# Optimization experiments

Hardware: AMD Instinct MI355X
Metric: run time of the kernel (lower is better)

Reference implementation:

```python
import jax, jax.numpy as jnp
import numpy as np

S = 4096      # sequence length
E = 256       # embedding_dim
H = 256       # hidden_dim // 2 (per direction)
T = 16        # tagset size
V = 100000    # vocab size
START = 14
STOP = 15
NEG = -10000.0


def setup_inputs() -> dict:
    key = jax.random.key(0)
    ks = jax.random.split(key, 16)
    trans = jax.random.normal(ks[12], (T, T), jnp.float32)
    trans = trans.at[START, :].set(NEG).at[:, STOP].set(NEG)
    return {
        "sentence": jax.random.randint(ks[0], (S,), 0, V),
        "embed": jax.random.normal(ks[1], (V, E), jnp.float32),
        "W_ih_f": jax.random.normal(ks[2], (4 * H, E), jnp.float32) * 0.05,
        "W_hh_f": jax.random.normal(ks[3], (4 * H, H), jnp.float32) * 0.05,
        "b_ih_f": jax.random.normal(ks[4], (4 * H,), jnp.float32) * 0.05,
        "b_hh_f": jax.random.normal(ks[5], (4 * H,), jnp.float32) * 0.05,
        "W_ih_b": jax.random.normal(ks[6], (4 * H, E), jnp.float32) * 0.05,
        "W_hh_b": jax.random.normal(ks[7], (4 * H, H), jnp.float32) * 0.05,
        "b_ih_b": jax.random.normal(ks[8], (4 * H,), jnp.float32) * 0.05,
        "b_hh_b": jax.random.normal(ks[9], (4 * H,), jnp.float32) * 0.05,
        "W_out": jax.random.normal(ks[10], (T, 2 * H), jnp.float32) * 0.05,
        "b_out": jax.random.normal(ks[11], (T,), jnp.float32) * 0.05,
        "transitions": trans,
        "h0": jax.random.normal(ks[13], (2, H), jnp.float32),
        "c0": jax.random.normal(ks[14], (2, H), jnp.float32),
    }


def _lstm(x, h0, c0, W_ih, W_hh, b_ih, b_hh):
    """Single-direction LSTM over x:[S,E]; PyTorch gate order i,f,g,o."""
    b = b_ih + b_hh
    xg = x @ W_ih.T + b  # [S, 4H] precompute input contribution

    def step(carry, xt):
        h, c = carry
        g = xt + h @ W_hh.T
        i, f, gg, o = jnp.split(g, 4)
        i = jax.nn.sigmoid(i)
        f = jax.nn.sigmoid(f)
        gg = jnp.tanh(gg)
        o = jax.nn.sigmoid(o)
        c = f * c + i * gg
        h = o * jnp.tanh(c)
        return (h, c), h

    _, hs = jax.lax.scan(step, (h0, c0), xg)
    return hs  # [S, H]


def reference(sentence, embed, W_ih_f, W_hh_f, b_ih_f, b_hh_f,
              W_ih_b, W_hh_b, b_ih_b, b_hh_b, W_out, b_out,
              transitions, h0, c0):
    x = embed[sentence]  # [S, E]
    hf = _lstm(x, h0[0], c0[0], W_ih_f, W_hh_f, b_ih_f, b_hh_f)
    hb = _lstm(x[::-1], h0[1], c0[1], W_ih_b, W_hh_b, b_ih_b, b_hh_b)[::-1]
    feats = jnp.concatenate([hf, hb], axis=-1) @ W_out.T + b_out  # [S, T]

    # CRF forward algorithm (log partition). transitions[i, j] = score j -> i.
    alpha0 = jnp.full((T,), NEG, feats.dtype).at[START].set(0.0)

    def crf_step(alpha, emit):
        a = jax.nn.logsumexp(alpha[None, :] + transitions, axis=1) + emit
        return a, None

    alpha, _ = jax.lax.scan(crf_step, alpha0, feats)
    return jax.nn.logsumexp(alpha + transitions[STOP])
```

## Files before the change

### kernel.cpp

```cpp
#include <hip/hip_runtime.h>
#include <hip/hip_bf16.h>

#define S 4096
#define E 256
#define HH 256
#define TT 16
#define NEG_ -10000.0f
#define START_ 14
#define STOP_ 15

__device__ __forceinline__ float fast_exp(float x) {
    return __builtin_amdgcn_exp2f(x * 1.4426950408889634f);
}
__device__ __forceinline__ float fast_log(float x) {
    return 0.6931471805599453f * __builtin_amdgcn_logf(x);
}

__global__ __launch_bounds__(64) void quant4_kernel(
    const float* __restrict__ Wf, const float* __restrict__ Wb,
    const float* __restrict__ h0,
    int* __restrict__ wq4, float* __restrict__ wscale,
    int* __restrict__ hq0p, float* __restrict__ sh0)
{
    int blk = blockIdx.x, lane = threadIdx.x;
    const float* src;
    int* dst;
    float* scl;
    bool fixed = false;
    if (blk < 2048) {
        int d = blk >> 10, r = blk & 1023;
        src = (d == 0 ? Wf : Wb) + (size_t)r * 256;
        dst = wq4 + ((size_t)(d * 1024 + r)) * 32;
        scl = wscale + (d * 1024 + r);
    } else {
        int d = blk - 2048;
        src = h0 + (size_t)d * 256;
        dst = hq0p + d * 32;
        scl = sh0 + d;
        fixed = true;
    }
    float4 a = make_float4(0.f, 0.f, 0.f, 0.f), b = a;
    if (lane < 32) {
        a = ((const float4*)src)[2 * lane];
        b = ((const float4*)src)[2 * lane + 1];
    }
    float f[8] = {a.x, a.y, a.z, a.w, b.x, b.y, b.z, b.w};
    float m = 0.f;
    #pragma unroll
    for (int k = 0; k < 8; ++k) m = fmaxf(m, fabsf(f[k]));
    #pragma unroll
    for (int off = 1; off < 64; off <<= 1) m = fmaxf(m, __shfl_xor(m, off, 64));
    m = fmaxf(m, 1e-20f);
    float inv = fixed ? 7.0f : (7.0f / m);
    if (lane < 32) {
        int dw = 0;
        #pragma unroll
        for (int k = 0; k < 8; ++k) {
            int q = __float2int_rn(f[k] * inv);
            q = max(-8, min(7, q));
            dw |= (q & 0xF) << (4 * k);
        }
        dst[lane] = dw;
    }
    if (lane == 0) *scl = fixed ? (1.0f / 7.0f) : (m / 7.0f);
}

__global__ __launch_bounds__(256) void xg_kernel(
    const int* __restrict__ sent, const float* __restrict__ embed,
    const float* __restrict__ Wf, const float* __restrict__ bihf, const float* __restrict__ bhhf,
    const float* __restrict__ Wb, const float* __restrict__ bihb, const float* __restrict__ bhhb,
    float* __restrict__ xg)
{
    const int dir = blockIdx.y;
    const int t0 = blockIdx.x * 16;
    const int tid = threadIdx.x;
    const float* W = dir ? Wb : Wf;
    __shared__ float xt[16][256];
    for (int tt = 0; tt < 16; ++tt) {
        int t = t0 + tt;
        int pos = dir ? (S - 1 - t) : t;
        int w = sent[pos];
        xt[tt][tid] = embed[(size_t)w * 256 + tid];
    }
    __syncthreads();
    float acc[4][16];
    #pragma unroll
    for (int rc = 0; rc < 4; ++rc)
        #pragma unroll
        for (int tt = 0; tt < 16; ++tt) acc[rc][tt] = 0.f;
    for (int e = 0; e < 256; ++e) {
        float xv[16];
        #pragma unroll
        for (int tt = 0; tt < 16; ++tt) xv[tt] = xt[tt][e];
        #pragma unroll
        for (int rc = 0; rc < 4; ++rc) {
            float w = W[(size_t)(rc * 256 + tid) * 256 + e];
            #pragma unroll
            for (int tt = 0; tt < 16; ++tt) acc[rc][tt] += w * xv[tt];
        }
    }
    const float* bih = dir ? bihb : bihf;
    const float* bhh = dir ? bhhb : bhhf;
    float b0 = bih[0 * 256 + tid] + bhh[0 * 256 + tid];
    float b1 = bih[1 * 256 + tid] + bhh[1 * 256 + tid];
    float b2 = bih[2 * 256 + tid] + bhh[2 * 256 + tid];
    float b3 = bih[3 * 256 + tid] + bhh[3 * 256 + tid];
    #pragma unroll
    for (int tt = 0; tt < 16; ++tt) {
        float4 v;
        v.x = acc[0][tt] + b0;
        v.y = acc[1][tt] + b1;
        v.z = acc[2][tt] + b2;
        v.w = acc[3][tt] + b3;
        ((float4*)(xg + ((size_t)dir * S + (t0 + tt)) * 1024))[tid] = v;
    }
}

#define D8(a,w,h) "v_dot8_i32_i4 " a ", " w ", " h ", " a "\n\t"
#define CH(H0,H1,H2,H3, I0,I1,I2,I3, F0,F1,F2,F3, G0,G1,G2,G3, O0,O1,O2,O3) \
 D8("v192",I0,H0) D8("v193",F0,H0) D8("v194",G0,H0) D8("v195",O0,H0) \
 D8("v192",I1,H1) D8("v193",F1,H1) D8("v194",G1,H1) D8("v195",O1,H1) \
 D8("v192",I2,H2) D8("v193",F2,H2) D8("v194",G2,H2) D8("v195",O2,H2) \
 D8("v192",I3,H3) D8("v193",F3,H3) D8("v194",G3,H3) D8("v195",O3,H3)

#define LSTM_BODY(XI, XF, XG, XO, NQUAD) \
  "global_load_dwordx4 " NQUAD ", v204, %[sxg]\n\t" \
  "ds_read_b128 v[160:163], v206\n\t" \
  "ds_read_b128 v[164:167], v206 offset:16\n\t" \
  "ds_read_b128 v[168:171], v206 offset:32\n\t" \
  "ds_read_b128 v[172:175], v206 offset:48\n\t" \
  "ds_read_b128 v[176:179], v206 offset:64\n\t" \
  "ds_read_b128 v[180:183], v206 offset:80\n\t" \
  "ds_read_b128 v[184:187], v206 offset:96\n\t" \
  "ds_read_b128 v[188:191], v206 offset:112\n\t" \
  "v_mov_b32 v192, 0\n\t" \
  "v_mov_b32 v193, 0\n\t" \
  "v_mov_b32 v194, 0\n\t" \
  "v_mov_b32 v195, 0\n\t" \
  "s_waitcnt lgkmcnt(7)\n\t" \
  CH("v160","v161","v162","v163", "v32","v33","v34","v35", "v64","v65","v66","v67", "v96","v97","v98","v99", "v128","v129","v130","v131") \
  "s_waitcnt lgkmcnt(6)\n\t" \
  CH("v164","v165","v166","v167", "v36","v37","v38","v39", "v68","v69","v70","v71", "v100","v101","v102","v103", "v132","v133","v134","v135") \
  "s_waitcnt lgkmcnt(5)\n\t" \
  CH("v168","v169","v170","v171", "v40","v41","v42","v43", "v72","v73","v74","v75", "v104","v105","v106","v107", "v136","v137","v138","v139") \
  "s_waitcnt lgkmcnt(4)\n\t" \
  CH("v172","v173","v174","v175", "v44","v45","v46","v47", "v76","v77","v78","v79", "v108","v109","v110","v111", "v140","v141","v142","v143") \
  "s_waitcnt lgkmcnt(3)\n\t" \
  CH("v176","v177","v178","v179", "v48","v49","v50","v51", "v80","v81","v82","v83", "v112","v113","v114","v115", "v144","v145","v146","v147") \
  "s_waitcnt lgkmcnt(2)\n\t" \
  CH("v180","v181","v182","v183", "v52","v53","v54","v55", "v84","v85","v86","v87", "v116","v117","v118","v119", "v148","v149","v150","v151") \
  "s_waitcnt lgkmcnt(1)\n\t" \
  CH("v184","v185","v186","v187", "v56","v57","v58","v59", "v88","v89","v90","v91", "v120","v121","v122","v123", "v152","v153","v154","v155") \
  "s_waitcnt lgkmcnt(0)\n\t" \
  CH("v188","v189","v190","v191", "v60","v61","v62","v63", "v92","v93","v94","v95", "v124","v125","v126","v127", "v156","v157","v158","v159") \
  "v_cvt_f32_i32 v208, v192\n\t" \
  "v_cvt_f32_i32 v209, v193\n\t" \
  "v_cvt_f32_i32 v210, v194\n\t" \
  "v_cvt_f32_i32 v211, v195\n\t" \
  "s_waitcnt vmcnt(2)\n\t" \
  "v_fma_f32 v212, %[sci], v208, " XI "\n\t" \
  "v_fma_f32 v213, %[scf], v209, " XF "\n\t" \
  "v_fma_f32 v214, %[scg], v210, " XG "\n\t" \
  "v_fma_f32 v215, %[sco], v211, " XO "\n\t" \
  "v_mul_f32 v208, %[nk], v212\n\t" \
  "v_mul_f32 v209, %[nk], v213\n\t" \
  "v_mul_f32 v211, %[nk], v215\n\t" \
  "v_med3_f32 v214, v214, %[ncl], %[pcl]\n\t" \
  "v_mul_f32 v210, %[k2], v214\n\t" \
  "v_exp_f32 v208, v208\n\t" \
  "v_exp_f32 v209, v209\n\t" \
  "v_exp_f32 v211, v211\n\t" \
  "v_exp_f32 v210, v210\n\t" \
  "s_nop 1\n\t" \
  "v_add_f32 v212, 1.0, v208\n\t" \
  "v_add_f32 v213, 1.0, v209\n\t" \
  "v_add_f32 v215, 1.0, v211\n\t" \
  "v_add_f32 v216, 1.0, v210\n\t" \
  "v_add_f32 v217, -1.0, v210\n\t" \
  "v_rcp_f32 v212, v212\n\t" \
  "v_rcp_f32 v213, v213\n\t" \
  "v_rcp_f32 v215, v215\n\t" \
  "v_rcp_f32 v216, v216\n\t" \
  "s_nop 1\n\t" \
  "v_mul_f32 v217, v217, v216\n\t" \
  "v_mul_f32 v220, v213, v220\n\t" \
  "v_fmac_f32 v220, v212, v217\n\t" \
  "v_med3_f32 v208, v220, %[ncl], %[pcl]\n\t" \
  "v_mul_f32 v208, %[k2], v208\n\t" \
  "v_exp_f32 v208, v208\n\t" \
  "s_nop 1\n\t" \
  "v_add_f32 v209, -1.0, v208\n\t" \
  "v_add_f32 v210, 1.0, v208\n\t" \
  "v_rcp_f32 v210, v210\n\t" \
  "s_nop 1\n\t" \
  "v_mul_f32 v209, v209, v210\n\t" \
  "v_mul_f32 v218, v215, v209\n\t" \
  "global_store_dword v205, v218, %[shs]\n\t" \
  "v_mul_f32 v208, %[c7], v218\n\t" \
  "v_rndne_f32 v208, v208\n\t" \
  "v_cvt_i32_f32 v208, v208\n\t" \
  "v_and_b32 v208, 15, v208\n\t" \
  "v_lshlrev_b32 v208, v225, v208\n\t" \
  "s_nop 1\n\t" \
  "v_mov_b32_dpp v209, v208 quad_perm:[1,0,3,2] row_mask:0xf bank_mask:0xf\n\t" \
  "v_or_b32 v208, v208, v209\n\t" \
  "s_nop 1\n\t" \
  "v_mov_b32_dpp v209, v208 quad_perm:[2,3,0,1] row_mask:0xf bank_mask:0xf\n\t" \
  "v_or_b32 v208, v208, v209\n\t" \
  "ds_write_b16 v207, v208\n\t" \
  "v_add_u32 v204, 0x1000, v204\n\t" \
  "v_add_u32 v205, 0x400, v205\n\t" \
  "v_xor_b32 v206, 0x80, v206\n\t" \
  "v_xor_b32 v207, 0x80, v207\n\t" \
  "s_waitcnt lgkmcnt(0)\n\t" \
  "s_barrier\n\t"

__global__ __launch_bounds__(256, 1) void lstm_kernel(
    const float* __restrict__ xg, const int* __restrict__ wq4,
    const float* __restrict__ wscale, const int* __restrict__ hq0p,
    const float* __restrict__ c0, float* __restrict__ hs)
{
    const int d = blockIdx.x;
    const int t = threadIdx.x;

    __shared__ alignas(16) int hq4buf[256];

    const int*   wq_d = wq4 + (size_t)d * 32768;
    const float* xg_d = xg + (size_t)d * S * 1024;
    float*       hs_d = hs + (size_t)d * S * 256;
    const float sci = wscale[d * 1024 + t]       * (1.0f / 7.0f);
    const float scf = wscale[d * 1024 + 256 + t] * (1.0f / 7.0f);
    const float scg = wscale[d * 1024 + 512 + t] * (1.0f / 7.0f);
    const float sco = wscale[d * 1024 + 768 + t] * (1.0f / 7.0f);
    const float c0v = c0[d * 256 + t];
    const int h0v = hq0p[d * 32 + (t & 31)];
    const unsigned h0a = (t < 32) ? (unsigned)t * 4u : (512u + (unsigned)(t & 63) * 4u);
    const unsigned xai = (unsigned)t * 16u;
    const unsigned hsi = (unsigned)t * 4u;
    const unsigned wad = ((t & 3) == 0) ? (128u + (unsigned)(t >> 1))
                                        : (512u + (unsigned)t * 2u);
    const unsigned voW = (unsigned)t * 128u;
    const unsigned shf = (unsigned)(t & 3) * 4u;
    const float nk = -1.4426950408889634f;
    const float k2 = 2.8853900817779268f;
    const float c7 = 7.0f;
    const float ncl = -30.0f, pcl = 30.0f;
    const unsigned lds_keep = (unsigned)(size_t)&hq4buf[0];
    int cnt = S / 2;

    asm volatile(
        "v_mov_b32 v204, %[xai]\n\t"
        "v_mov_b32 v205, %[hsi]\n\t"
        "v_mov_b32 v206, 0\n\t"
        "v_mov_b32 v207, %[wad]\n\t"
        "v_mov_b32 v220, %[c0v]\n\t"
        "v_mov_b32 v221, %[sci]\n\t"
        "v_mov_b32 v222, %[scf]\n\t"
        "v_mov_b32 v223, %[scg]\n\t"
        "v_mov_b32 v224, %[sco]\n\t"
        "v_mov_b32 v225, %[shf]\n\t"
        "ds_write_b32 %[h0a], %[h0v]\n\t"
        "v_mov_b32 v208, %[voW]\n\t"
        "global_load_dwordx4 v[32:35], v208, %[swq]\n\t"
        "global_load_dwordx4 v[36:39], v208, %[swq] offset:16\n\t"
        "global_load_dwordx4 v[40:43], v208, %[swq] offset:32\n\t"
        "global_load_dwordx4 v[44:47], v208, %[swq] offset:48\n\t"
        "global_load_dwordx4 v[48:51], v208, %[swq] offset:64\n\t"
        "global_load_dwordx4 v[52:55], v208, %[swq] offset:80\n\t"
        "global_load_dwordx4 v[56:59], v208, %[swq] offset:96\n\t"
        "global_load_dwordx4 v[60:63], v208, %[swq] offset:112\n\t"
        "v_add_u32 v208, 0x8000, v208\n\t"
        "global_load_dwordx4 v[64:67], v208, %[swq]\n\t"
        "global_load_dwordx4 v[68:71], v208, %[swq] offset:16\n\t"
        "global_load_dwordx4 v[72:75], v208, %[swq] offset:32\n\t"
        "global_load_dwordx4 v[76:79], v208, %[swq] offset:48\n\t"
        "global_load_dwordx4 v[80:83], v208, %[swq] offset:64\n\t"
        "global_load_dwordx4 v[84:87], v208, %[swq] offset:80\n\t"
        "global_load_dwordx4 v[88:91], v208, %[swq] offset:96\n\t"
        "global_load_dwordx4 v[92:95], v208, %[swq] offset:112\n\t"
        "v_add_u32 v208, 0x8000, v208\n\t"
        "global_load_dwordx4 v[96:99],   v208, %[swq]\n\t"
        "global_load_dwordx4 v[100:103], v208, %[swq] offset:16\n\t"
        "global_load_dwordx4 v[104:107], v208, %[swq] offset:32\n\t"
        "global_load_dwordx4 v[108:111], v208, %[swq] offset:48\n\t"
        "global_load_dwordx4 v[112:115], v208, %[swq] offset:64\n\t"
        "global_load_dwordx4 v[116:119], v208, %[swq] offset:80\n\t"
        "global_load_dwordx4 v[120:123], v208, %[swq] offset:96\n\t"
        "global_load_dwordx4 v[124:127], v208, %[swq] offset:112\n\t"
        "v_add_u32 v208, 0x8000, v208\n\t"
        "global_load_dwordx4 v[128:131], v208, %[swq]\n\t"
        "global_load_dwordx4 v[132:135], v208, %[swq] offset:16\n\t"
        "global_load_dwordx4 v[136:139], v208, %[swq] offset:32\n\t"
        "global_load_dwordx4 v[140:143], v208, %[swq] offset:48\n\t"
        "global_load_dwordx4 v[144:147], v208, %[swq] offset:64\n\t"
        "global_load_dwordx4 v[148:151], v208, %[swq] offset:80\n\t"
        "global_load_dwordx4 v[152:155], v208, %[swq] offset:96\n\t"
        "global_load_dwordx4 v[156:159], v208, %[swq] offset:112\n\t"
        "global_load_dwordx4 v[196:199], v204, %[sxg]\n\t"
        "v_add_u32 v204, 0x1000, v204\n\t"
        "s_waitcnt vmcnt(0) lgkmcnt(0)\n\t"
        "s_barrier\n\t"
        "Llstm%=:\n\t"
        LSTM_BODY("v196", "v197", "v198", "v199", "v[200:203]")
        LSTM_BODY("v200", "v201", "v202", "v203", "v[196:199]")
        "s_add_i32 %[cnt], %[cnt], -1\n\t"
        "s_cmp_lg_u32 %[cnt], 0\n\t"
        "s_cbranch_scc1 Llstm%=\n\t"
        : [cnt] "+s"(cnt)
        : [sxg] "s"(xg_d), [shs] "s"(hs_d), [swq] "s"(wq_d),
          [xai] "v"(xai), [hsi] "v"(hsi), [wad] "v"(wad),
          [c0v] "v"(c0v), [h0a] "v"(h0a), [h0v] "v"(h0v),
          [sci] "v"(sci), [scf] "v"(scf), [scg] "v"(scg), [sco] "v"(sco),
          [nk] "v"(nk), [k2] "v"(k2), [c7] "v"(c7),
          [ncl] "v"(ncl), [pcl] "v"(pcl),
          [voW] "v"(voW), [shf] "v"(shf), [keep] "v"(lds_keep)
        : "memory", "scc",
          "v32","v33","v34","v35","v36","v37","v38","v39",
          "v40","v41","v42","v43","v44","v45","v46","v47",
          "v48","v49","v50","v51","v52","v53","v54","v55",
          "v56","v57","v58","v59","v60","v61","v62","v63",
          "v64","v65","v66","v67","v68","v69","v70","v71",
          "v72","v73","v74","v75","v76","v77","v78","v79",
          "v80","v81","v82","v83","v84","v85","v86","v87",
          "v88","v89","v90","v91","v92","v93","v94","v95",
          "v96","v97","v98","v99","v100","v101","v102","v103",
          "v104","v105","v106","v107","v108","v109","v110","v111",
          "v112","v113","v114","v115","v116","v117","v118","v119",
          "v120","v121","v122","v123","v124","v125","v126","v127",
          "v128","v129","v130","v131","v132","v133","v134","v135",
          "v136","v137","v138","v139","v140","v141","v142","v143",
          "v144","v145","v146","v147","v148","v149","v150","v151",
          "v152","v153","v154","v155","v156","v157","v158","v159",
          "v160","v161","v162","v163","v164","v165","v166","v167",
          "v168","v169","v170","v171","v172","v173","v174","v175",
          "v176","v177","v178","v179","v180","v181","v182","v183",
          "v184","v185","v186","v187","v188","v189","v190","v191",
          "v192","v193","v194","v195","v196","v197","v198","v199",
          "v200","v201","v202","v203","v204","v205","v206","v207",
          "v208","v209","v210","v211","v212","v213","v214","v215",
          "v216","v217","v218","v219","v220","v221","v222","v223",
          "v224","v225");
}

__global__ __launch_bounds__(256) void feats_kernel(
    const float* __restrict__ hs, const float* __restrict__ Wout,
    const float* __restrict__ bout, float* __restrict__ feats)
{
    __shared__ float Wl[16][513];
    int tid = threadIdx.x;
    for (int i = tid; i < 16 * 512; i += 256) Wl[i >> 9][i & 511] = Wout[i];
    __syncthreads();
    int tt = tid >> 4, tag = tid & 15;
    int tcur = blockIdx.x * 16 + tt;
    const float* hf = hs + (size_t)tcur * 256;
    const float* hb = hs + (size_t)S * 256 + (size_t)(S - 1 - tcur) * 256;
    float acc = bout[tag];
    for (int k = 0; k < 256; ++k) acc += Wl[tag][k] * hf[k];
    for (int k = 0; k < 256; ++k) acc += Wl[tag][256 + k] * hb[k];
    feats[(size_t)tcur * 16 + tag] = acc;
}

__global__ __launch_bounds__(256) void crf_chunk_kernel(
    const float* __restrict__ feats, const float* __restrict__ trans,
    float* __restrict__ P)
{
    int chunk = blockIdx.x;
    int tid = threadIdx.x;
    int i = tid >> 4, jj = tid & 15;
    __shared__ float Mt[2][16][17];
    float tr[16];
    #pragma unroll
    for (int k = 0; k < 16; ++k) tr[k] = trans[i * 16 + k];
    int t0 = chunk * 64;
    float emit = feats[(size_t)t0 * 16 + i];
    Mt[0][jj][i] = tr[jj] + emit;
    __syncthreads();
    int cur = 0;
    float em_next = feats[(size_t)(t0 + 1) * 16 + i];
    for (int s = 1; s < 64; ++s) {
        float em = em_next;
        if (s + 1 < 64) em_next = feats[(size_t)(t0 + s + 1) * 16 + i];
        float v[16];
        #pragma unroll
        for (int k = 0; k < 16; ++k) v[k] = tr[k] + Mt[cur][jj][k];
        float m = v[0];
        #pragma unroll
        for (int k = 1; k < 16; ++k) m = fmaxf(m, v[k]);
        float ssum = 0.f;
        #pragma unroll
        for (int k = 0; k < 16; ++k) ssum += fast_exp(v[k] - m);
        float nv = em + m + fast_log(ssum);
        Mt[cur ^ 1][jj][i] = nv;
        cur ^= 1;
        __syncthreads();
    }
    P[((size_t)chunk * 16 + i) * 16 + jj] = Mt[cur][jj][i];
}

__global__ __launch_bounds__(256) void crf_fold_kernel(
    const float* __restrict__ P, const float* __restrict__ trans,
    float* __restrict__ out)
{
    int tid = threadIdx.x;
    int i = tid >> 4, jj = tid & 15;
    __shared__ float alpha[16];
    if (tid < 16) alpha[tid] = (tid == START_) ? 0.0f : NEG_;
    __syncthreads();
    for (int cc = 0; cc < 64; ++cc) {
        float pv = P[((size_t)cc * 16 + i) * 16 + jj];
        float v = pv + alpha[jj];
        float m = v;
        #pragma unroll
        for (int off = 1; off < 16; off <<= 1) m = fmaxf(m, __shfl_xor(m, off, 64));
        float e = fast_exp(v - m);
        #pragma unroll
        for (int off = 1; off < 16; off <<= 1) e += __shfl_xor(e, off, 64);
        float nv = m + fast_log(e);
        __syncthreads();
        if (jj == 0) alpha[i] = nv;
        __syncthreads();
    }
    if (tid < 16) {
        float v = alpha[tid] + trans[STOP_ * 16 + tid];
        float m = v;
        #pragma unroll
        for (int off = 1; off < 16; off <<= 1) m = fmaxf(m, __shfl_xor(m, off, 64));
        float e = fast_exp(v - m);
        #pragma unroll
        for (int off = 1; off < 16; off <<= 1) e += __shfl_xor(e, off, 64);
        if (tid == 0) out[0] = m + fast_log(e);
    }
}

extern "C" void kernel_launch(void* const* d_in, const int* in_sizes, int n_in,
                              void* d_out, int out_size, void* d_ws, size_t ws_size,
                              hipStream_t stream) {
    const int*   sent  = (const int*)d_in[0];
    const float* embed = (const float*)d_in[1];
    const float* Wihf  = (const float*)d_in[2];
    const float* Whhf  = (const float*)d_in[3];
    const float* bihf  = (const float*)d_in[4];
    const float* bhhf  = (const float*)d_in[5];
    const float* Wihb  = (const float*)d_in[6];
    const float* Whhb  = (const float*)d_in[7];
    const float* bihb  = (const float*)d_in[8];
    const float* bhhb  = (const float*)d_in[9];
    const float* Wout  = (const float*)d_in[10];
    const float* bout  = (const float*)d_in[11];
    const float* trans = (const float*)d_in[12];
    const float* h0    = (const float*)d_in[13];
    const float* c0    = (const float*)d_in[14];
    float* out = (float*)d_out;

    char* ws = (char*)d_ws;
    constexpr size_t OFF_XG     = 0;
    constexpr size_t OFF_WQ     = OFF_XG + (size_t)2 * S * 1024 * 4;
    constexpr size_t OFF_WSCALE = OFF_WQ + (size_t)2 * 1024 * 32 * 4;
    constexpr size_t OFF_HQ0    = OFF_WSCALE + 2 * 1024 * 4;
    constexpr size_t OFF_SH0    = OFF_HQ0 + 2 * 32 * 4;
    constexpr size_t OFF_HS     = OFF_SH0 + 256;
    constexpr size_t OFF_FEATS  = OFF_HS + (size_t)2 * S * 256 * 4;
    constexpr size_t OFF_P      = OFF_FEATS + (size_t)S * 16 * 4;

    float* xg     = (float*)(ws + OFF_XG);
    int*   wq4    = (int*)(ws + OFF_WQ);
    float* wscale = (float*)(ws + OFF_WSCALE);
    int*   hq0p   = (int*)(ws + OFF_HQ0);
    float* sh0    = (float*)(ws + OFF_SH0);
    float* hs     = (float*)(ws + OFF_HS);
    float* feats  = (float*)(ws + OFF_FEATS);
    float* P      = (float*)(ws + OFF_P);

    quant4_kernel<<<dim3(2050), dim3(64), 0, stream>>>(Whhf, Whhb, h0, wq4, wscale, hq0p, sh0);
    xg_kernel<<<dim3(256, 2), dim3(256), 0, stream>>>(sent, embed, Wihf, bihf, bhhf,
                                                      Wihb, bihb, bhhb, xg);
    lstm_kernel<<<dim3(2), dim3(256), 0, stream>>>(xg, wq4, wscale, hq0p, c0, hs);
    feats_kernel<<<dim3(256), dim3(256), 0, stream>>>(hs, Wout, bout, feats);
    crf_chunk_kernel<<<dim3(64), dim3(256), 0, stream>>>(feats, trans, P);
    crf_fold_kernel<<<dim3(1), dim3(256), 0, stream>>>(P, trans, out);
}
```

Measured before the change: 2.362 ms.

## Defer hidden-state store, double-buffer LDS h, and transpose W_ih for coalesced xg

The LSTM step loop is rescheduled. The global store of h and the xg prefetch move to the top of the next iteration, the LDS h buffer is double-buffered so reads and writes alternate, and accumulator zeroing moves off the critical path. Hidden-state quantisation now uses a magic-number add instead of rndne plus cvt, and the output arrays get a one-row offset to absorb the delayed store. A new transpose kernel makes W_ih reads in xg_kernel coalesced, at the cost of an extra launch and scratch buffer.

```diff
diff --git a/kernel.cpp b/kernel.cpp
--- a/kernel.cpp
+++ b/kernel.cpp
@@ -8,6 +8,7 @@
 #define NEG_ -10000.0f
 #define START_ 14
 #define STOP_ 15
+#define DSTRIDE_F (S * 256 + 256)
 
 __device__ __forceinline__ float fast_exp(float x) {
     return __builtin_amdgcn_exp2f(x * 1.4426950408889634f);
@@ -20,12 +21,12 @@
     const float* __restrict__ Wf, const float* __restrict__ Wb,
     const float* __restrict__ h0,
     int* __restrict__ wq4, float* __restrict__ wscale,
-    int* __restrict__ hq0p, float* __restrict__ sh0)
+    int* __restrict__ hq0p)
 {
     int blk = blockIdx.x, lane = threadIdx.x;
     const float* src;
     int* dst;
-    float* scl;
+    float* scl = nullptr;
     bool fixed = false;
     if (blk < 2048) {
         int d = blk >> 10, r = blk & 1023;
@@ -36,7 +37,6 @@
         int d = blk - 2048;
         src = h0 + (size_t)d * 256;
         dst = hq0p + d * 32;
-        scl = sh0 + d;
         fixed = true;
     }
     float4 a = make_float4(0.f, 0.f, 0.f, 0.f), b = a;
@@ -62,19 +62,39 @@
         }
         dst[lane] = dw;
     }
-    if (lane == 0) *scl = fixed ? (1.0f / 7.0f) : (m / 7.0f);
+    if (!fixed && lane == 0) *scl = m / 7.0f;
+}
+
+__global__ __launch_bounds__(256) void transpose_kernel(
+    const float* __restrict__ Wf, const float* __restrict__ Wb,
+    float* __restrict__ WT)
+{
+    __shared__ float tile[32][33];
+    const int dir = blockIdx.z;
+    const float* W = dir ? Wb : Wf;
+    const int r0 = blockIdx.x * 32, e0 = blockIdx.y * 32;
+    const int tr = threadIdx.x & 31, tc = threadIdx.x >> 5;
+    #pragma unroll
+    for (int i = 0; i < 32; i += 8)
+        tile[tc + i][tr] = W[(size_t)(r0 + tc + i) * 256 + e0 + tr];
+    __syncthreads();
+    float* out = WT + (size_t)dir * 256 * 1024;
+    #pragma unroll
+    for (int i = 0; i < 32; i += 8)
+        out[(size_t)(e0 + tc + i) * 1024 + r0 + tr] = tile[tr][tc + i];
 }
 
 __global__ __launch_bounds__(256) void xg_kernel(
     const int* __restrict__ sent, const float* __restrict__ embed,
-    const float* __restrict__ Wf, const float* __restrict__ bihf, const float* __restrict__ bhhf,
-    const float* __restrict__ Wb, const float* __restrict__ bihb, const float* __restrict__ bhhb,
+    const float* __restrict__ WT,
+    const float* __restrict__ bihf, const float* __restrict__ bhhf,
+    const float* __restrict__ bihb, const float* __restrict__ bhhb,
     float* __restrict__ xg)
 {
     const int dir = blockIdx.y;
     const int t0 = blockIdx.x * 16;
     const int tid = threadIdx.x;
-    const float* W = dir ? Wb : Wf;
+    const float* Wt = WT + (size_t)dir * 256 * 1024;
     __shared__ float xt[16][256];
     for (int tt = 0; tt < 16; ++tt) {
         int t = t0 + tt;
@@ -92,9 +112,10 @@
         float xv[16];
         #pragma unroll
         for (int tt = 0; tt < 16; ++tt) xv[tt] = xt[tt][e];
+        const float* wrow = Wt + (size_t)e * 1024;
         #pragma unroll
         for (int rc = 0; rc < 4; ++rc) {
-            float w = W[(size_t)(rc * 256 + tid) * 256 + e];
+            float w = wrow[rc * 256 + tid];
             #pragma unroll
             for (int tt = 0; tt < 16; ++tt) acc[rc][tt] += w * xv[tt];
         }
@@ -124,7 +145,6 @@
  D8("v192",I3,H3) D8("v193",F3,H3) D8("v194",G3,H3) D8("v195",O3,H3)
 
 #define LSTM_BODY(XI, XF, XG, XO, NQUAD) \
-  "global_load_dwordx4 " NQUAD ", v204, %[sxg]\n\t" \
   "ds_read_b128 v[160:163], v206\n\t" \
   "ds_read_b128 v[164:167], v206 offset:16\n\t" \
   "ds_read_b128 v[168:171], v206 offset:32\n\t" \
@@ -133,10 +153,11 @@
   "ds_read_b128 v[180:183], v206 offset:80\n\t" \
   "ds_read_b128 v[184:187], v206 offset:96\n\t" \
   "ds_read_b128 v[188:191], v206 offset:112\n\t" \
-  "v_mov_b32 v192, 0\n\t" \
-  "v_mov_b32 v193, 0\n\t" \
-  "v_mov_b32 v194, 0\n\t" \
-  "v_mov_b32 v195, 0\n\t" \
+  "v_xor_b32 v206, 0x80, v206\n\t" \
+  "global_store_dword v205, v218, %[shs]\n\t" \
+  "v_add_u32 v205, 0x400, v205\n\t" \
+  "global_load_dwordx4 " NQUAD ", v204, %[sxg]\n\t" \
+  "v_add_u32 v204, 0x1000, v204\n\t" \
   "s_waitcnt lgkmcnt(7)\n\t" \
   CH("v160","v161","v162","v163", "v32","v33","v34","v35", "v64","v65","v66","v67", "v96","v97","v98","v99", "v128","v129","v130","v131") \
   "s_waitcnt lgkmcnt(6)\n\t" \
@@ -183,6 +204,7 @@
   "v_rcp_f32 v216, v216\n\t" \
   "s_nop 1\n\t" \
   "v_mul_f32 v217, v217, v216\n\t" \
+  "v_mul_f32 v219, %[c7], v215\n\t" \
   "v_mul_f32 v220, v213, v220\n\t" \
   "v_fmac_f32 v220, v212, v217\n\t" \
   "v_med3_f32 v208, v220, %[ncl], %[pcl]\n\t" \
@@ -194,13 +216,11 @@
   "v_rcp_f32 v210, v210\n\t" \
   "s_nop 1\n\t" \
   "v_mul_f32 v209, v209, v210\n\t" \
-  "v_mul_f32 v218, v215, v209\n\t" \
-  "global_store_dword v205, v218, %[shs]\n\t" \
-  "v_mul_f32 v208, %[c7], v218\n\t" \
-  "v_rndne_f32 v208, v208\n\t" \
-  "v_cvt_i32_f32 v208, v208\n\t" \
+  "v_mul_f32 v217, v219, v209\n\t" \
+  "v_add_f32 v208, 0x4b400000, v217\n\t" \
   "v_and_b32 v208, 15, v208\n\t" \
   "v_lshlrev_b32 v208, v225, v208\n\t" \
+  "v_mul_f32 v218, %[i7], v217\n\t" \
   "s_nop 1\n\t" \
   "v_mov_b32_dpp v209, v208 quad_perm:[1,0,3,2] row_mask:0xf bank_mask:0xf\n\t" \
   "v_or_b32 v208, v208, v209\n\t" \
@@ -208,10 +228,11 @@
   "v_mov_b32_dpp v209, v208 quad_perm:[2,3,0,1] row_mask:0xf bank_mask:0xf\n\t" \
   "v_or_b32 v208, v208, v209\n\t" \
   "ds_write_b16 v207, v208\n\t" \
-  "v_add_u32 v204, 0x1000, v204\n\t" \
-  "v_add_u32 v205, 0x400, v205\n\t" \
-  "v_xor_b32 v206, 0x80, v206\n\t" \
   "v_xor_b32 v207, 0x80, v207\n\t" \
+  "v_mov_b32 v192, 0\n\t" \
+  "v_mov_b32 v193, 0\n\t" \
+  "v_mov_b32 v194, 0\n\t" \
+  "v_mov_b32 v195, 0\n\t" \
   "s_waitcnt lgkmcnt(0)\n\t" \
   "s_barrier\n\t"
 
@@ -223,27 +244,28 @@
     const int d = blockIdx.x;
     const int t = threadIdx.x;
 
-    __shared__ alignas(16) int hq4buf[256];
+    __shared__ alignas(16) int hq4buf[512];
 
     const int*   wq_d = wq4 + (size_t)d * 32768;
     const float* xg_d = xg + (size_t)d * S * 1024;
-    float*       hs_d = hs + (size_t)d * S * 256;
+    float*       hs_d = hs + (size_t)d * DSTRIDE_F;
     const float sci = wscale[d * 1024 + t]       * (1.0f / 7.0f);
     const float scf = wscale[d * 1024 + 256 + t] * (1.0f / 7.0f);
     const float scg = wscale[d * 1024 + 512 + t] * (1.0f / 7.0f);
     const float sco = wscale[d * 1024 + 768 + t] * (1.0f / 7.0f);
     const float c0v = c0[d * 256 + t];
     const int h0v = hq0p[d * 32 + (t & 31)];
-    const unsigned h0a = (t < 32) ? (unsigned)t * 4u : (512u + (unsigned)(t & 63) * 4u);
+    const unsigned h0a = (t < 32) ? (unsigned)t * 4u : (1536u + (unsigned)(t & 63) * 4u);
     const unsigned xai = (unsigned)t * 16u;
     const unsigned hsi = (unsigned)t * 4u;
     const unsigned wad = ((t & 3) == 0) ? (128u + (unsigned)(t >> 1))
-                                        : (512u + (unsigned)t * 2u);
+                                        : (512u + (unsigned)((t & 255) << 2));
     const unsigned voW = (unsigned)t * 128u;
     const unsigned shf = (unsigned)(t & 3) * 4u;
     const float nk = -1.4426950408889634f;
     const float k2 = 2.8853900817779268f;
     const float c7 = 7.0f;
+    const float i7 = 1.0f / 7.0f;
     const float ncl = -30.0f, pcl = 30.0f;
     const unsigned lds_keep = (unsigned)(size_t)&hq4buf[0];
     int cnt = S / 2;
@@ -253,12 +275,13 @@
         "v_mov_b32 v205, %[hsi]\n\t"
         "v_mov_b32 v206, 0\n\t"
         "v_mov_b32 v207, %[wad]\n\t"
+        "v_mov_b32 v218, 0\n\t"
         "v_mov_b32 v220, %[c0v]\n\t"
-        "v_mov_b32 v221, %[sci]\n\t"
-        "v_mov_b32 v222, %[scf]\n\t"
-        "v_mov_b32 v223, %[scg]\n\t"
-        "v_mov_b32 v224, %[sco]\n\t"
         "v_mov_b32 v225, %[shf]\n\t"
+        "v_mov_b32 v192, 0\n\t"
+        "v_mov_b32 v193, 0\n\t"
+        "v_mov_b32 v194, 0\n\t"
+        "v_mov_b32 v195, 0\n\t"
         "ds_write_b32 %[h0a], %[h0v]\n\t"
         "v_mov_b32 v208, %[voW]\n\t"
         "global_load_dwordx4 v[32:35], v208, %[swq]\n\t"
@@ -306,12 +329,13 @@
         "s_add_i32 %[cnt], %[cnt], -1\n\t"
         "s_cmp_lg_u32 %[cnt], 0\n\t"
         "s_cbranch_scc1 Llstm%=\n\t"
+        "global_store_dword v205, v218, %[shs]\n\t"
         : [cnt] "+s"(cnt)
         : [sxg] "s"(xg_d), [shs] "s"(hs_d), [swq] "s"(wq_d),
           [xai] "v"(xai), [hsi] "v"(hsi), [wad] "v"(wad),
           [c0v] "v"(c0v), [h0a] "v"(h0a), [h0v] "v"(h0v),
           [sci] "v"(sci), [scf] "v"(scf), [scg] "v"(scg), [sco] "v"(sco),
-          [nk] "v"(nk), [k2] "v"(k2), [c7] "v"(c7),
+          [nk] "v"(nk), [k2] "v"(k2), [c7] "v"(c7), [i7] "v"(i7),
           [ncl] "v"(ncl), [pcl] "v"(pcl),
           [voW] "v"(voW), [shf] "v"(shf), [keep] "v"(lds_keep)
         : "memory", "scc",
@@ -343,7 +367,8 @@
 }
 
 __global__ __launch_bounds__(256) void feats_kernel(
-    const float* __restrict__ hs, const float* __restrict__ Wout,
+    const float* __restrict__ hsf, const float* __restrict__ hsb,
+    const float* __restrict__ Wout,
     const float* __restrict__ bout, float* __restrict__ feats)
 {
     __shared__ float Wl[16][513];
@@ -352,8 +377,8 @@
     __syncthreads();
     int tt = tid >> 4, tag = tid & 15;
     int tcur = blockIdx.x * 16 + tt;
-    const float* hf = hs + (size_t)tcur * 256;
-    const float* hb = hs + (size_t)S * 256 + (size_t)(S - 1 - tcur) * 256;
+    const float* hf = hsf + (size_t)tcur * 256;
+    const float* hb = hsb + (size_t)(S - 1 - tcur) * 256;
     float acc = bout[tag];
     for (int k = 0; k < 256; ++k) acc += Wl[tag][k] * hf[k];
     for (int k = 0; k < 256; ++k) acc += Wl[tag][256 + k] * hb[k];
@@ -457,25 +482,27 @@
     constexpr size_t OFF_WQ     = OFF_XG + (size_t)2 * S * 1024 * 4;
     constexpr size_t OFF_WSCALE = OFF_WQ + (size_t)2 * 1024 * 32 * 4;
     constexpr size_t OFF_HQ0    = OFF_WSCALE + 2 * 1024 * 4;
-    constexpr size_t OFF_SH0    = OFF_HQ0 + 2 * 32 * 4;
-    constexpr size_t OFF_HS     = OFF_SH0 + 256;
-    constexpr size_t OFF_FEATS  = OFF_HS + (size_t)2 * S * 256 * 4;
+    constexpr size_t OFF_WT     = OFF_HQ0 + 256;
+    constexpr size_t OFF_HS     = OFF_WT + (size_t)2 * 256 * 1024 * 4;
+    constexpr size_t OFF_FEATS  = OFF_HS + (size_t)2 * DSTRIDE_F * 4;
     constexpr size_t OFF_P      = OFF_FEATS + (size_t)S * 16 * 4;
 
     float* xg     = (float*)(ws + OFF_XG);
     int*   wq4    = (int*)(ws + OFF_WQ);
     float* wscale = (float*)(ws + OFF_WSCALE);
     int*   hq0p   = (int*)(ws + OFF_HQ0);
-    float* sh0    = (float*)(ws + OFF_SH0);
+    float* WT     = (float*)(ws + OFF_WT);
     float* hs     = (float*)(ws + OFF_HS);
     float* feats  = (float*)(ws + OFF_FEATS);
     float* P      = (float*)(ws + OFF_P);
 
-    quant4_kernel<<<dim3(2050), dim3(64), 0, stream>>>(Whhf, Whhb, h0, wq4, wscale, hq0p, sh0);
-    xg_kernel<<<dim3(256, 2), dim3(256), 0, stream>>>(sent, embed, Wihf, bihf, bhhf,
-                                                      Wihb, bihb, bhhb, xg);
+    quant4_kernel<<<dim3(2050), dim3(64), 0, stream>>>(Whhf, Whhb, h0, wq4, wscale, hq0p);
+    transpose_kernel<<<dim3(32, 8, 2), dim3(256), 0, stream>>>(Wihf, Wihb, WT);
+    xg_kernel<<<dim3(256, 2), dim3(256), 0, stream>>>(sent, embed, WT, bihf, bhhf,
+                                                      bihb, bhhb, xg);
     lstm_kernel<<<dim3(2), dim3(256), 0, stream>>>(xg, wq4, wscale, hq0p, c0, hs);
-    feats_kernel<<<dim3(256), dim3(256), 0, stream>>>(hs, Wout, bout, feats);
+    feats_kernel<<<dim3(256), dim3(256), 0, stream>>>(hs + 256, hs + DSTRIDE_F + 256,
+                                                      Wout, bout, feats);
     crf_chunk_kernel<<<dim3(64), dim3(256), 0, stream>>>(feats, trans, P);
     crf_fold_kernel<<<dim3(1), dim3(256), 0, stream>>>(P, trans, out);
 }
```

After: 2.154 ms (median of 2 runs). 8.8% less time.
